# Kernel optimization log

Measured on AMD Instinct MI355X. Metric: run time of the kernel, lower is better.

## Reference

```python
import jax, jax.numpy as jnp
import numpy as np
from jax import lax

B = 256
WIDTH = 64
STRUCT = [512, 1024, 1024, 1000]
N_LAYERS = len(STRUCT) - 2  # LSTM layers (last pair is the classifier)


def setup_inputs() -> dict:
    key = jax.random.key(0)
    ks = list(jax.random.split(key, 2 + 4 * N_LAYERS))
    inp = {"x": jax.random.normal(ks[0], (B, STRUCT[0] * WIDTH), jnp.float32)}
    ki = 1
    for j in range(N_LAYERS):
        n_x, n_h = STRUCT[j], STRUCT[j + 1]
        n_v = n_h + n_x  # variants == 0: concat(h_prev, x)
        std = np.float32(np.sqrt(2.0 / (n_v + n_h)))
        for g in ["F", "I", "C", "O"]:
            inp[f"{g}{j}"] = jax.random.normal(ks[ki], (n_v, n_h), jnp.float32) * std
            ki += 1
        for g in ["bf", "bi", "bc", "bo"]:
            inp[f"{g}{j}"] = jnp.zeros((n_h,), jnp.float32)
    n_x, n_h = STRUCT[-2], STRUCT[-1]
    std = np.float32(np.sqrt(2.0 / (n_x + n_h)))
    inp["W"] = jax.random.normal(ks[ki], (n_x, n_h), jnp.float32) * std
    inp["b"] = jnp.zeros((n_h,), jnp.float32)
    return inp


def _lstm_forward(x, params, W, b):
    # x: [B, WIDTH*n_in] -> xs: [WIDTH, B, n_in] (tf.split along axis 1)
    bsz = x.shape[0]
    xs = x.reshape(bsz, WIDTH, STRUCT[0]).transpose(1, 0, 2)

    def step(carry, x_t):
        new_carry = []
        h = x_t
        for j, (F, I, C, O, bf, bi, bc, bo) in enumerate(params):
            c_f, h_f = carry[j]
            # variants==0: x_in = concat([h_prev, x]); k==0 sliced-weight path
            # equals zero h_prev/c_prev, so zero-init state is faithful.
            x_in = jnp.concatenate([h_f, h], axis=1)  # [B, n_h + n_x]
            f = jax.nn.sigmoid(x_in @ F + bf)
            i = jax.nn.sigmoid(x_in @ I + bi)
            c = f * c_f + i * jnp.tanh(x_in @ C + bc)
            o = jax.nn.sigmoid(x_in @ O + bo)
            h = o * jnp.tanh(c)
            new_carry.append((c, h))
        return tuple(new_carry), None

    init = tuple(
        (jnp.zeros((bsz, STRUCT[j + 1]), x.dtype), jnp.zeros((bsz, STRUCT[j + 1]), x.dtype))
        for j in range(N_LAYERS)
    )
    carry, _ = lax.scan(step, init, xs)
    h_last = carry[-1][1]  # top layer hidden at final timestep
    logits = h_last @ W + b
    pred = jax.nn.softmax(logits, axis=-1)
    return logits, pred


def reference(x, F0, I0, C0, O0, bf0, bi0, bc0, bo0,
              F1, I1, C1, O1, bf1, bi1, bc1, bo1, W, b):
    params = [
        (F0, I0, C0, O0, bf0, bi0, bc0, bo0),
        (F1, I1, C1, O1, bf1, bi1, bc1, bo1),
    ]
    return _lstm_forward(x, params, W, b)
```

## Files before the change

### kernel.cpp

```cpp
#include <hip/hip_runtime.h>
#include <hip/hip_bf16.h>


typedef short  bf16x8 __attribute__((ext_vector_type(8)));
typedef float  f32x4  __attribute__((ext_vector_type(4)));

#define NHID   1024
#define NBATCH 256
#define NBLK   256
#define HSZE   (NBATCH * NHID)

__device__ __forceinline__ unsigned short f2b(float f) {
    unsigned int u = __builtin_bit_cast(unsigned int, f);
    unsigned int r = (u + 0x7FFFu + ((u >> 16) & 1u)) >> 16;
    return (unsigned short)r;
}
__device__ __forceinline__ float sigmoidf_(float x) {
    return 1.0f / (1.0f + __expf(-x));
}
__device__ __forceinline__ float tanhf_(float x) {
    return 1.0f - 2.0f / (__expf(2.0f * x) + 1.0f);
}

__global__ __launch_bounds__(256)
void transpose_w_kernel(const float* __restrict__ w0, const float* __restrict__ w1,
                        const float* __restrict__ w2, const float* __restrict__ w3,
                        unsigned short* __restrict__ dst, int nv) {
    __shared__ unsigned short t[64][65];
    const int gate = blockIdx.z;
    const float* src = (gate == 0) ? w0 : (gate == 1) ? w1 : (gate == 2) ? w2 : w3;
    const int kt = blockIdx.x * 64;
    const int nt = blockIdx.y * 64;
    const int tid = threadIdx.x;
    const int rr = tid >> 6;
    const int cc = tid & 63;
    #pragma unroll
    for (int p = 0; p < 16; ++p) {
        const int row = p * 4 + rr;
        t[cc][row] = f2b(src[(size_t)(kt + row) * NHID + nt + cc]);
    }
    __syncthreads();
    #pragma unroll
    for (int p = 0; p < 16; ++p) {
        const int row = p * 4 + rr;
        dst[((size_t)gate * NHID + nt + row) * nv + kt + cc] = t[row][cc];
    }
}

__global__ __launch_bounds__(256)
void cvt_x_frag_kernel(const float* __restrict__ x, unsigned short* __restrict__ xb) {
    const int t  = blockIdx.x;
    const int mg = blockIdx.y;
    const int g  = threadIdx.x >> 6;
    const int l  = threadIdx.x & 63;
    const int row = l & 15, ko = l >> 4;
    const float* src = x + (size_t)(mg * 16 + row) * 32768 + t * 512 + ko * 8;
    unsigned short* dst = xb + ((size_t)t * 256 * 512) + ((size_t)mg * 16 * 64 + l) * 8;
    #pragma unroll
    for (int i = 0; i < 4; ++i) {
        const int c = g * 4 + i;
        const float4 v0 = *(const float4*)(src + (size_t)c * 32);
        const float4 v1 = *(const float4*)(src + (size_t)c * 32 + 4);
        ushort4 o0, o1;
        o0.x = f2b(v0.x); o0.y = f2b(v0.y); o0.z = f2b(v0.z); o0.w = f2b(v0.w);
        o1.x = f2b(v1.x); o1.y = f2b(v1.y); o1.z = f2b(v1.z); o1.w = f2b(v1.w);
        *(ushort4*)(dst + (size_t)c * 512)     = o0;
        *(ushort4*)(dst + (size_t)c * 512 + 4) = o1;
    }
}

__device__ __forceinline__ void grid_sync(unsigned* bar, unsigned gen) {
    __syncthreads();
    if (threadIdx.x == 0) {
        __builtin_amdgcn_fence(__ATOMIC_RELEASE, "agent");
        unsigned* grp  = bar + (blockIdx.x & 7) * 16;
        unsigned* glob = bar + 128;
        unsigned* gctr = bar + 144;
        if (__hip_atomic_fetch_add(grp, 1u, __ATOMIC_RELAXED, __HIP_MEMORY_SCOPE_AGENT)
                == gen * 32u + 31u) {
            if (__hip_atomic_fetch_add(glob, 1u, __ATOMIC_RELAXED, __HIP_MEMORY_SCOPE_AGENT)
                    == gen * 8u + 7u) {
                __hip_atomic_store(gctr, gen + 1u, __ATOMIC_RELAXED, __HIP_MEMORY_SCOPE_AGENT);
            }
        }
        while (__hip_atomic_load(gctr, __ATOMIC_RELAXED, __HIP_MEMORY_SCOPE_AGENT) <= gen) {
            __builtin_amdgcn_s_sleep(2);
        }
        __builtin_amdgcn_fence(__ATOMIC_ACQUIRE, "agent");
    }
    __syncthreads();
}

__global__ __launch_bounds__(512)
void lstm_persist_kernel(const unsigned short* __restrict__ wt0,
                         const unsigned short* __restrict__ wt1,
                         const unsigned short* __restrict__ xb,
                         const float* __restrict__ bf0, const float* __restrict__ bi0,
                         const float* __restrict__ bc0, const float* __restrict__ bo0,
                         const float* __restrict__ bf1, const float* __restrict__ bi1,
                         const float* __restrict__ bc1, const float* __restrict__ bo1,
                         unsigned short* __restrict__ h0b,
                         unsigned short* __restrict__ h1b,
                         float* __restrict__ h1f,
                         unsigned* __restrict__ bar) {
    __shared__ __align__(16) unsigned short lw[65536];

    const int tid  = threadIdx.x;
    const int lane = tid & 63;
    const int w    = tid >> 6;
    const int c15  = lane & 15;
    const int kg   = lane >> 4;
    const int b    = blockIdx.x;
    const int layer = (b >> 3) & 1;
    const int lb    = ((b >> 4) << 3) | (b & 7);

    const unsigned short* wt = layer ? wt1 : wt0;
    const int NV  = layer ? 2048 : 1536;
    const int NCW = NV >> 5;
    const int NX  = layer ? 32 : 16;

    #pragma unroll
    for (int i = 0; i < 8; ++i) {
        const int c = w + i * 8;
        if (c < NCW) {
            #pragma unroll
            for (int rt = 0; rt < 2; ++rt) {
                const int R   = rt * 16 + c15;
                const int g   = R >> 3;
                const int hid = 8 * lb + (R & 7);
                const int k   = c * 32 + kg * 8;
                *(bf16x8*)(lw + ((size_t)(c * 2 + rt) * 64 + lane) * 8) =
                    *(const bf16x8*)(wt + ((size_t)g * NHID + hid) * NV + k);
            }
        }
    }

    f32x4 biasv[2];
    {
        const float* bp[4];
        if (layer) { bp[0] = bf1; bp[1] = bi1; bp[2] = bc1; bp[3] = bo1; }
        else       { bp[0] = bf0; bp[1] = bi0; bp[2] = bc0; bp[3] = bo0; }
        #pragma unroll
        for (int rt = 0; rt < 2; ++rt)
            #pragma unroll
            for (int j = 0; j < 4; ++j) {
                const int R = rt * 16 + kg * 4 + j;
                biasv[rt][j] = bp[R >> 3][8 * lb + (R & 7)];
            }
    }
    __syncthreads();

    float cs[4] = {0.f, 0.f, 0.f, 0.f};
    unsigned gen = 0;

    const int rot_h = (b >> 3) & 31;
    const int rot_x = layer ? rot_h : ((b >> 4) & 15);
    const bool hiM  = (kg >= 2);

    const int chw = lb >> 2, kow = lb & 3, eb = (kg & 1) * 4;
    const int mg   = 2 * w + (hiM ? 1 : 0);
    const int mrow = 32 * w + (hiM ? 16 : 0) + c15;
    const size_t hoff = (((size_t)mg * 32 + chw) * 64 + kow * 16 + c15) * 8 + eb;

    auto step = [&](const unsigned short* bh, const unsigned short* bx,
                    unsigned short* hout, float* hfout) {
        f32x4 a00 = biasv[0], a01 = biasv[0];
        f32x4 a10 = biasv[1], a11 = biasv[1];
        const unsigned short* ph0 = bh + ((size_t)(2 * w)     * 32 * 64 + lane) * 8;
        const unsigned short* ph1 = bh + ((size_t)(2 * w + 1) * 32 * 64 + lane) * 8;
        const unsigned short* px0 = bx + ((size_t)(2 * w)     * NX * 64 + lane) * 8;
        const unsigned short* px1 = bx + ((size_t)(2 * w + 1) * NX * 64 + lane) * 8;

        #pragma unroll 8
        for (int i = 0; i < 32; ++i) {
            const int cc = (i + rot_h) & 31;
            const bf16x8 va0 = *(const bf16x8*)(lw + ((size_t)(cc * 2)     * 64 + lane) * 8);
            const bf16x8 va1 = *(const bf16x8*)(lw + ((size_t)(cc * 2 + 1) * 64 + lane) * 8);
            const bf16x8 vb0 = *(const bf16x8*)(ph0 + (size_t)cc * 512);
            const bf16x8 vb1 = *(const bf16x8*)(ph1 + (size_t)cc * 512);
            a00 = __builtin_amdgcn_mfma_f32_16x16x32_bf16(va0, vb0, a00, 0, 0, 0);
            a01 = __builtin_amdgcn_mfma_f32_16x16x32_bf16(va0, vb1, a01, 0, 0, 0);
            a10 = __builtin_amdgcn_mfma_f32_16x16x32_bf16(va1, vb0, a10, 0, 0, 0);
            a11 = __builtin_amdgcn_mfma_f32_16x16x32_bf16(va1, vb1, a11, 0, 0, 0);
        }
        #pragma unroll 8
        for (int i = 0; i < NX; ++i) {
            const int cc = (i + rot_x) & (NX - 1);
            const bf16x8 va0 = *(const bf16x8*)(lw + ((size_t)((32 + cc) * 2)     * 64 + lane) * 8);
            const bf16x8 va1 = *(const bf16x8*)(lw + ((size_t)((32 + cc) * 2 + 1) * 64 + lane) * 8);
            const bf16x8 vb0 = *(const bf16x8*)(px0 + (size_t)cc * 512);
            const bf16x8 vb1 = *(const bf16x8*)(px1 + (size_t)cc * 512);
            a00 = __builtin_amdgcn_mfma_f32_16x16x32_bf16(va0, vb0, a00, 0, 0, 0);
            a01 = __builtin_amdgcn_mfma_f32_16x16x32_bf16(va0, vb1, a01, 0, 0, 0);
            a10 = __builtin_amdgcn_mfma_f32_16x16x32_bf16(va1, vb0, a10, 0, 0, 0);
            a11 = __builtin_amdgcn_mfma_f32_16x16x32_bf16(va1, vb1, a11, 0, 0, 0);
        }

        f32x4 r0, r1;
        #pragma unroll
        for (int j = 0; j < 4; ++j) {
            const float s0 = hiM ? a01[j] : a00[j];
            const float s1 = hiM ? a11[j] : a10[j];
            const float t0 = __shfl_xor(a00[j], 32);
            const float t1 = __shfl_xor(a01[j], 32);
            const float t2 = __shfl_xor(a10[j], 32);
            const float t3 = __shfl_xor(a11[j], 32);
            r0[j] = hiM ? t1 : t0;
            r1[j] = hiM ? t3 : t2;
            (void)s0; (void)s1;
        }
        const f32x4 own0 = hiM ? a01 : a00;
        const f32x4 own1 = hiM ? a11 : a10;

        ushort4 hb;
        float4  hf;
        float hv[4];
        #pragma unroll
        for (int j = 0; j < 4; ++j) {
            const float fsv = hiM ? r0[j]   : own0[j];
            const float isv = hiM ? own0[j] : r0[j];
            const float csv = hiM ? r1[j]   : own1[j];
            const float osv = hiM ? own1[j] : r1[j];
            const float fv = sigmoidf_(fsv);
            const float iv = sigmoidf_(isv);
            const float cv = tanhf_(csv);
            const float ov = sigmoidf_(osv);
            const float ccv = fv * cs[j] + iv * cv;
            const float hh  = ov * tanhf_(ccv);
            cs[j] = ccv;
            hv[j] = hh;
        }
        hb.x = f2b(hv[0]); hb.y = f2b(hv[1]); hb.z = f2b(hv[2]); hb.w = f2b(hv[3]);
        *reinterpret_cast<ushort4*>(hout + hoff) = hb;
        if (hfout) {
            hf.x = hv[0]; hf.y = hv[1]; hf.z = hv[2]; hf.w = hv[3];
            *reinterpret_cast<float4*>(hfout + (size_t)mrow * NHID + 8 * lb + eb) = hf;
        }
    };

    for (int t = 0; t <= 64; ++t) {
        if (layer == 0) {
            if (t < 64) {
                step(h0b + (size_t)((t + 1) & 1) * HSZE,
                     xb + (size_t)t * 256 * 512,
                     h0b + (size_t)(t & 1) * HSZE, nullptr);
            }
        } else {
            if (t >= 1) {
                const int u = t - 1;
                step(h1b + (size_t)((u + 1) & 1) * HSZE,
                     h0b + (size_t)(u & 1) * HSZE,
                     h1b + (size_t)(u & 1) * HSZE,
                     (u == 63) ? h1f : nullptr);
            }
        }
        if (t < 64) {
            grid_sync(bar, gen);
            ++gen;
        }
    }
}

__global__ __launch_bounds__(256)
void classifier_kernel(const float* __restrict__ h, const float* __restrict__ W,
                       const float* __restrict__ b, float* __restrict__ logits) {
    __shared__ float hs[4 * 1024];
    const int tid = threadIdx.x;
    const int m0 = blockIdx.y * 4;
    const int n  = blockIdx.x * 256 + tid;
    #pragma unroll
    for (int i = 0; i < 16; ++i)
        hs[i * 256 + tid] = h[(size_t)m0 * NHID + i * 256 + tid];
    __syncthreads();
    if (n < 1000) {
        float a0 = 0.f, a1 = 0.f, a2 = 0.f, a3 = 0.f;
        #pragma unroll 8
        for (int k = 0; k < NHID; ++k) {
            const float wv = W[(size_t)k * 1000 + n];
            a0 = fmaf(hs[k], wv, a0);
            a1 = fmaf(hs[1024 + k], wv, a1);
            a2 = fmaf(hs[2048 + k], wv, a2);
            a3 = fmaf(hs[3072 + k], wv, a3);
        }
        const float bv = b[n];
        logits[(size_t)(m0 + 0) * 1000 + n] = a0 + bv;
        logits[(size_t)(m0 + 1) * 1000 + n] = a1 + bv;
        logits[(size_t)(m0 + 2) * 1000 + n] = a2 + bv;
        logits[(size_t)(m0 + 3) * 1000 + n] = a3 + bv;
    }
}

__global__ void softmax_kernel(const float* __restrict__ logits, float* __restrict__ pred) {
    __shared__ float red[256];
    const int m = blockIdx.x;
    const int t = threadIdx.x;
    const float* lr = logits + (size_t)m * 1000;
    float mx = -3.4e38f;
    for (int i = t; i < 1000; i += 256) mx = fmaxf(mx, lr[i]);
    red[t] = mx; __syncthreads();
    for (int off = 128; off > 0; off >>= 1) {
        if (t < off) red[t] = fmaxf(red[t], red[t + off]);
        __syncthreads();
    }
    mx = red[0];
    __syncthreads();
    float sm = 0.0f;
    for (int i = t; i < 1000; i += 256) sm += __expf(lr[i] - mx);
    red[t] = sm; __syncthreads();
    for (int off = 128; off > 0; off >>= 1) {
        if (t < off) red[t] += red[t + off];
        __syncthreads();
    }
    const float inv = 1.0f / red[0];
    for (int i = t; i < 1000; i += 256)
        pred[(size_t)m * 1000 + i] = __expf(lr[i] - mx) * inv;
}

extern "C" void kernel_launch(void* const* d_in, const int* in_sizes, int n_in,
                              void* d_out, int out_size, void* d_ws, size_t ws_size,
                              hipStream_t stream) {
    (void)in_sizes; (void)n_in; (void)out_size; (void)ws_size;
    const float* x = (const float*)d_in[0];
    const float* W0[4] = {(const float*)d_in[1], (const float*)d_in[2], (const float*)d_in[3], (const float*)d_in[4]};
    const float* B0[4] = {(const float*)d_in[5], (const float*)d_in[6], (const float*)d_in[7], (const float*)d_in[8]};
    const float* W1[4] = {(const float*)d_in[9], (const float*)d_in[10], (const float*)d_in[11], (const float*)d_in[12]};
    const float* B1[4] = {(const float*)d_in[13], (const float*)d_in[14], (const float*)d_in[15], (const float*)d_in[16]};
    const float* Wc = (const float*)d_in[17];
    const float* bc = (const float*)d_in[18];
    float* out = (float*)d_out;

    char* ws = (char*)d_ws;
    size_t off = 0;
    auto alloc = [&](size_t bytes) -> char* {
        char* p = ws + off;
        off += (bytes + 255) & ~(size_t)255;
        return p;
    };
    unsigned short* wt0 = (unsigned short*)alloc((size_t)4 * NHID * 1536 * 2);
    unsigned short* wt1 = (unsigned short*)alloc((size_t)4 * NHID * 2048 * 2);
    unsigned short* xb  = (unsigned short*)alloc((size_t)NBATCH * 64 * 512 * 2);
    char* hstates = ws + off;
    unsigned short* h0b = (unsigned short*)alloc((size_t)2 * HSZE * 2);
    unsigned short* h1b = (unsigned short*)alloc((size_t)2 * HSZE * 2);
    size_t hstate_bytes = (size_t)((char*)h1b + (size_t)2 * HSZE * 2 - hstates);
    float* h1f = (float*)alloc((size_t)HSZE * 4);
    unsigned* bar = (unsigned*)alloc(1024);

    hipMemsetAsync(hstates, 0, hstate_bytes, stream);
    hipMemsetAsync(bar, 0, 1024, stream);

    transpose_w_kernel<<<dim3(1536 / 64, 16, 4), 256, 0, stream>>>(
        W0[0], W0[1], W0[2], W0[3], wt0, 1536);
    transpose_w_kernel<<<dim3(2048 / 64, 16, 4), 256, 0, stream>>>(
        W1[0], W1[1], W1[2], W1[3], wt1, 2048);
    cvt_x_frag_kernel<<<dim3(64, 16), 256, 0, stream>>>(x, xb);

    lstm_persist_kernel<<<NBLK, 512, 0, stream>>>(
        wt0, wt1, xb,
        B0[0], B0[1], B0[2], B0[3],
        B1[0], B1[1], B1[2], B1[3],
        h0b, h1b, h1f, bar);

    classifier_kernel<<<dim3(4, 64), 256, 0, stream>>>(h1f, Wc, bc, out);
    softmax_kernel<<<NBATCH, 256, 0, stream>>>(out, out + (size_t)NBATCH * 1000);
}
```

Before: 1.488 ms.

## Split LSTM persistent kernel across 512 blocks with four hidden units each

Doubles the persistent grid from 256 to 512 blocks. Each block now owns 4 hidden units per gate instead of 8, which halves the LDS weight slice (64 KB) and the MFMA work per block. The gate exchange is reworked to a two-stage lane shuffle, and the grid barrier now uses 16 groups. The aim is to spread the recurrent GEMV over more CUs and shorten each timestep's critical path. The cost is more blocks in every grid sync, a heavier atomic barrier, and a requirement that all 512 blocks be co-resident, which the added launch_bounds occupancy hint targets.

```diff
diff --git a/kernel.cpp b/kernel.cpp
--- a/kernel.cpp
+++ b/kernel.cpp
@@ -7,7 +7,6 @@
 
 #define NHID   1024
 #define NBATCH 256
-#define NBLK   256
 #define HSZE   (NBATCH * NHID)
 
 __device__ __forceinline__ unsigned short f2b(float f) {
@@ -73,13 +72,13 @@
     __syncthreads();
     if (threadIdx.x == 0) {
         __builtin_amdgcn_fence(__ATOMIC_RELEASE, "agent");
-        unsigned* grp  = bar + (blockIdx.x & 7) * 16;
-        unsigned* glob = bar + 128;
-        unsigned* gctr = bar + 144;
+        unsigned* grp  = bar + (blockIdx.x & 15) * 16;
+        unsigned* glob = bar + 256;
+        unsigned* gctr = bar + 272;
         if (__hip_atomic_fetch_add(grp, 1u, __ATOMIC_RELAXED, __HIP_MEMORY_SCOPE_AGENT)
                 == gen * 32u + 31u) {
             if (__hip_atomic_fetch_add(glob, 1u, __ATOMIC_RELAXED, __HIP_MEMORY_SCOPE_AGENT)
-                    == gen * 8u + 7u) {
+                    == gen * 16u + 15u) {
                 __hip_atomic_store(gctr, gen + 1u, __ATOMIC_RELAXED, __HIP_MEMORY_SCOPE_AGENT);
             }
         }
@@ -91,7 +90,7 @@
     __syncthreads();
 }
 
-__global__ __launch_bounds__(512)
+__global__ __launch_bounds__(512, 4)
 void lstm_persist_kernel(const unsigned short* __restrict__ wt0,
                          const unsigned short* __restrict__ wt1,
                          const unsigned short* __restrict__ xb,
@@ -103,7 +102,7 @@
                          unsigned short* __restrict__ h1b,
                          float* __restrict__ h1f,
                          unsigned* __restrict__ bar) {
-    __shared__ __align__(16) unsigned short lw[65536];
+    __shared__ __align__(16) unsigned short lw[32768];
 
     const int tid  = threadIdx.x;
     const int lane = tid & 63;
@@ -117,55 +116,48 @@
     const unsigned short* wt = layer ? wt1 : wt0;
     const int NV  = layer ? 2048 : 1536;
     const int NCW = NV >> 5;
-    const int NX  = layer ? 32 : 16;
-
-    #pragma unroll
-    for (int i = 0; i < 8; ++i) {
-        const int c = w + i * 8;
-        if (c < NCW) {
-            #pragma unroll
-            for (int rt = 0; rt < 2; ++rt) {
-                const int R   = rt * 16 + c15;
-                const int g   = R >> 3;
-                const int hid = 8 * lb + (R & 7);
-                const int k   = c * 32 + kg * 8;
-                *(bf16x8*)(lw + ((size_t)(c * 2 + rt) * 64 + lane) * 8) =
-                    *(const bf16x8*)(wt + ((size_t)g * NHID + hid) * NV + k);
-            }
-        }
-    }
-
-    f32x4 biasv[2];
+
     {
-        const float* bp[4];
-        if (layer) { bp[0] = bf1; bp[1] = bi1; bp[2] = bc1; bp[3] = bo1; }
-        else       { bp[0] = bf0; bp[1] = bi0; bp[2] = bc0; bp[3] = bo0; }
+        const int g   = c15 >> 2;
+        const int hid = 4 * lb + (c15 & 3);
+        const unsigned short* s = wt + ((size_t)g * NHID + hid) * NV + kg * 8;
         #pragma unroll
-        for (int rt = 0; rt < 2; ++rt)
-            #pragma unroll
-            for (int j = 0; j < 4; ++j) {
-                const int R = rt * 16 + kg * 4 + j;
-                biasv[rt][j] = bp[R >> 3][8 * lb + (R & 7)];
-            }
-    }
-    __syncthreads();
-
-    float cs[4] = {0.f, 0.f, 0.f, 0.f};
+        for (int i = 0; i < 8; ++i) {
+            const int c = w + i * 8;
+            if (c < NCW)
+                *(bf16x8*)(lw + ((size_t)c * 64 + lane) * 8) = *(const bf16x8*)(s + c * 32);
+        }
+    }
+
+    f32x4 biasv;
+    {
+        const float* bg;
+        if (layer) bg = (kg == 0) ? bf1 : (kg == 1) ? bi1 : (kg == 2) ? bc1 : bo1;
+        else       bg = (kg == 0) ? bf0 : (kg == 1) ? bi0 : (kg == 2) ? bc0 : bo0;
+        const float4 v = *(const float4*)(bg + 4 * lb);
+        biasv[0] = v.x; biasv[1] = v.y; biasv[2] = v.z; biasv[3] = v.w;
+    }
+    __syncthreads();
+
+    float cs[2] = {0.f, 0.f};
     unsigned gen = 0;
 
-    const int rot_h = (b >> 3) & 31;
-    const int rot_x = layer ? rot_h : ((b >> 4) & 15);
-    const bool hiM  = (kg >= 2);
-
-    const int chw = lb >> 2, kow = lb & 3, eb = (kg & 1) * 4;
-    const int mg   = 2 * w + (hiM ? 1 : 0);
-    const int mrow = 32 * w + (hiM ? 16 : 0) + c15;
-    const size_t hoff = (((size_t)mg * 32 + chw) * 64 + kow * 16 + c15) * 8 + eb;
-
-    auto step = [&](const unsigned short* bh, const unsigned short* bx,
+    const int rot_h  = (b >> 4) & 31;
+    const int rot_xL = layer ? ((b >> 4) & 31) : ((b >> 4) & 15);
+
+    const int mf = (kg >> 1) & 1;
+    const int jp = 2 * (kg & 1);
+    const int mg   = 2 * w + mf;
+    const int mrow = 32 * w + 16 * mf + c15;
+    const int chw  = lb >> 3;
+    const int kow  = (lb >> 1) & 3;
+    const int eoff = 4 * (lb & 1) + jp;
+    const size_t hoff = (((size_t)mg * 32 + chw) * 64 + kow * 16 + c15) * 8 + eoff;
+
+    auto step = [&](const int NX, const int rot_x,
+                    const unsigned short* bh, const unsigned short* bx,
                     unsigned short* hout, float* hfout) {
-        f32x4 a00 = biasv[0], a01 = biasv[0];
-        f32x4 a10 = biasv[1], a11 = biasv[1];
+        f32x4 acc0 = biasv, acc1 = biasv;
         const unsigned short* ph0 = bh + ((size_t)(2 * w)     * 32 * 64 + lane) * 8;
         const unsigned short* ph1 = bh + ((size_t)(2 * w + 1) * 32 * 64 + lane) * 8;
         const unsigned short* px0 = bx + ((size_t)(2 * w)     * NX * 64 + lane) * 8;
@@ -174,81 +166,77 @@
         #pragma unroll 8
         for (int i = 0; i < 32; ++i) {
             const int cc = (i + rot_h) & 31;
-            const bf16x8 va0 = *(const bf16x8*)(lw + ((size_t)(cc * 2)     * 64 + lane) * 8);
-            const bf16x8 va1 = *(const bf16x8*)(lw + ((size_t)(cc * 2 + 1) * 64 + lane) * 8);
-            const bf16x8 vb0 = *(const bf16x8*)(ph0 + (size_t)cc * 512);
-            const bf16x8 vb1 = *(const bf16x8*)(ph1 + (size_t)cc * 512);
-            a00 = __builtin_amdgcn_mfma_f32_16x16x32_bf16(va0, vb0, a00, 0, 0, 0);
-            a01 = __builtin_amdgcn_mfma_f32_16x16x32_bf16(va0, vb1, a01, 0, 0, 0);
-            a10 = __builtin_amdgcn_mfma_f32_16x16x32_bf16(va1, vb0, a10, 0, 0, 0);
-            a11 = __builtin_amdgcn_mfma_f32_16x16x32_bf16(va1, vb1, a11, 0, 0, 0);
+            const bf16x8 va = *(const bf16x8*)(lw + ((size_t)cc * 64 + lane) * 8);
+            const bf16x8 b0 = *(const bf16x8*)(ph0 + (size_t)cc * 512);
+            const bf16x8 b1 = *(const bf16x8*)(ph1 + (size_t)cc * 512);
+            acc0 = __builtin_amdgcn_mfma_f32_16x16x32_bf16(va, b0, acc0, 0, 0, 0);
+            acc1 = __builtin_amdgcn_mfma_f32_16x16x32_bf16(va, b1, acc1, 0, 0, 0);
         }
         #pragma unroll 8
         for (int i = 0; i < NX; ++i) {
             const int cc = (i + rot_x) & (NX - 1);
-            const bf16x8 va0 = *(const bf16x8*)(lw + ((size_t)((32 + cc) * 2)     * 64 + lane) * 8);
-            const bf16x8 va1 = *(const bf16x8*)(lw + ((size_t)((32 + cc) * 2 + 1) * 64 + lane) * 8);
-            const bf16x8 vb0 = *(const bf16x8*)(px0 + (size_t)cc * 512);
-            const bf16x8 vb1 = *(const bf16x8*)(px1 + (size_t)cc * 512);
-            a00 = __builtin_amdgcn_mfma_f32_16x16x32_bf16(va0, vb0, a00, 0, 0, 0);
-            a01 = __builtin_amdgcn_mfma_f32_16x16x32_bf16(va0, vb1, a01, 0, 0, 0);
-            a10 = __builtin_amdgcn_mfma_f32_16x16x32_bf16(va1, vb0, a10, 0, 0, 0);
-            a11 = __builtin_amdgcn_mfma_f32_16x16x32_bf16(va1, vb1, a11, 0, 0, 0);
-        }
-
-        f32x4 r0, r1;
+            const bf16x8 va = *(const bf16x8*)(lw + ((size_t)(32 + cc) * 64 + lane) * 8);
+            const bf16x8 b0 = *(const bf16x8*)(px0 + (size_t)cc * 512);
+            const bf16x8 b1 = *(const bf16x8*)(px1 + (size_t)cc * 512);
+            acc0 = __builtin_amdgcn_mfma_f32_16x16x32_bf16(va, b0, acc0, 0, 0, 0);
+            acc1 = __builtin_amdgcn_mfma_f32_16x16x32_bf16(va, b1, acc1, 0, 0, 0);
+        }
+
+        f32x4 sendA = (kg & 2) ? acc0 : acc1;
+        f32x4 recvA;
         #pragma unroll
-        for (int j = 0; j < 4; ++j) {
-            const float s0 = hiM ? a01[j] : a00[j];
-            const float s1 = hiM ? a11[j] : a10[j];
-            const float t0 = __shfl_xor(a00[j], 32);
-            const float t1 = __shfl_xor(a01[j], 32);
-            const float t2 = __shfl_xor(a10[j], 32);
-            const float t3 = __shfl_xor(a11[j], 32);
-            r0[j] = hiM ? t1 : t0;
-            r1[j] = hiM ? t3 : t2;
-            (void)s0; (void)s1;
-        }
-        const f32x4 own0 = hiM ? a01 : a00;
-        const f32x4 own1 = hiM ? a11 : a10;
-
-        ushort4 hb;
-        float4  hf;
-        float hv[4];
+        for (int j = 0; j < 4; ++j) recvA[j] = __shfl_xor(sendA[j], 32);
+        const f32x4 mine = (kg & 2) ? acc1 : acc0;
+
+        const int jo = 2 * ((kg & 1) ^ 1);
+        const float g1_0 = __shfl_xor(mine[jo],      16);
+        const float g1_1 = __shfl_xor(mine[jo + 1],  16);
+        const float g3_0 = __shfl_xor(recvA[jo],     16);
+        const float g3_1 = __shfl_xor(recvA[jo + 1], 16);
+        const float m_0  = mine[jp],  m_1  = mine[jp + 1];
+        const float rA_0 = recvA[jp], rA_1 = recvA[jp + 1];
+
+        float hv[2];
         #pragma unroll
-        for (int j = 0; j < 4; ++j) {
-            const float fsv = hiM ? r0[j]   : own0[j];
-            const float isv = hiM ? own0[j] : r0[j];
-            const float csv = hiM ? r1[j]   : own1[j];
-            const float osv = hiM ? own1[j] : r1[j];
+        for (int jj = 0; jj < 2; ++jj) {
+            const float m_  = jj ? m_1  : m_0;
+            const float g1  = jj ? g1_1 : g1_0;
+            const float rA  = jj ? rA_1 : rA_0;
+            const float g3  = jj ? g3_1 : g3_0;
+            const float fsv = (kg == 0) ? m_ : (kg == 1) ? g1 : (kg == 2) ? rA : g3;
+            const float isv = (kg == 1) ? m_ : (kg == 0) ? g1 : (kg == 3) ? rA : g3;
+            const float csv = (kg == 2) ? m_ : (kg == 3) ? g1 : (kg == 0) ? rA : g3;
+            const float osv = (kg == 3) ? m_ : (kg == 2) ? g1 : (kg == 1) ? rA : g3;
             const float fv = sigmoidf_(fsv);
             const float iv = sigmoidf_(isv);
             const float cv = tanhf_(csv);
             const float ov = sigmoidf_(osv);
-            const float ccv = fv * cs[j] + iv * cv;
+            const float ccv = fv * cs[jj] + iv * cv;
             const float hh  = ov * tanhf_(ccv);
-            cs[j] = ccv;
-            hv[j] = hh;
-        }
-        hb.x = f2b(hv[0]); hb.y = f2b(hv[1]); hb.z = f2b(hv[2]); hb.w = f2b(hv[3]);
-        *reinterpret_cast<ushort4*>(hout + hoff) = hb;
+            cs[jj] = ccv;
+            hv[jj] = hh;
+        }
+        const unsigned hb = (unsigned)f2b(hv[0]) | ((unsigned)f2b(hv[1]) << 16);
+        *reinterpret_cast<unsigned*>(hout + hoff) = hb;
         if (hfout) {
-            hf.x = hv[0]; hf.y = hv[1]; hf.z = hv[2]; hf.w = hv[3];
-            *reinterpret_cast<float4*>(hfout + (size_t)mrow * NHID + 8 * lb + eb) = hf;
+            float2 hf; hf.x = hv[0]; hf.y = hv[1];
+            *reinterpret_cast<float2*>(hfout + (size_t)mrow * NHID + 4 * lb + jp) = hf;
         }
     };
 
     for (int t = 0; t <= 64; ++t) {
         if (layer == 0) {
             if (t < 64) {
-                step(h0b + (size_t)((t + 1) & 1) * HSZE,
+                step(16, rot_xL,
+                     h0b + (size_t)((t + 1) & 1) * HSZE,
                      xb + (size_t)t * 256 * 512,
                      h0b + (size_t)(t & 1) * HSZE, nullptr);
             }
         } else {
             if (t >= 1) {
                 const int u = t - 1;
-                step(h1b + (size_t)((u + 1) & 1) * HSZE,
+                step(32, rot_xL,
+                     h1b + (size_t)((u + 1) & 1) * HSZE,
                      h0b + (size_t)(u & 1) * HSZE,
                      h1b + (size_t)(u & 1) * HSZE,
                      (u == 63) ? h1f : nullptr);
@@ -344,10 +332,10 @@
     unsigned short* h1b = (unsigned short*)alloc((size_t)2 * HSZE * 2);
     size_t hstate_bytes = (size_t)((char*)h1b + (size_t)2 * HSZE * 2 - hstates);
     float* h1f = (float*)alloc((size_t)HSZE * 4);
-    unsigned* bar = (unsigned*)alloc(1024);
+    unsigned* bar = (unsigned*)alloc(2048);
 
     hipMemsetAsync(hstates, 0, hstate_bytes, stream);
-    hipMemsetAsync(bar, 0, 1024, stream);
+    hipMemsetAsync(bar, 0, 2048, stream);
 
     transpose_w_kernel<<<dim3(1536 / 64, 16, 4), 256, 0, stream>>>(
         W0[0], W0[1], W0[2], W0[3], wt0, 1536);
@@ -355,7 +343,7 @@
         W1[0], W1[1], W1[2], W1[3], wt1, 2048);
     cvt_x_frag_kernel<<<dim3(64, 16), 256, 0, stream>>>(x, xb);
 
-    lstm_persist_kernel<<<NBLK, 512, 0, stream>>>(
+    lstm_persist_kernel<<<512, 512, 0, stream>>>(
         wt0, wt1, xb,
         B0[0], B0[1], B0[2], B0[3],
         B1[0], B1[1], B1[2], B1[3],
```

Measured after the change: 2.497 ms. 1.68x slower.

## Double threads per block, each wave computing one 16-row batch tile

Applied to the files above, without the earlier changes.

The persistent LSTM kernel now launches 1024 threads per block instead of 512. Each of the 16 waves handles one 16-row batch slice with two MFMA accumulators, where each of the 8 waves previously handled two slices with four. The aim is more waves per CU to hide latency on the serial per-timestep chain and a shorter MFMA chain per wave. In exchange, each weight fragment read from LDS is reused across half as many batch columns, LDS traffic per block roughly doubles, and the cell-update work is now split so each lane keeps two cell states instead of four.

```diff
diff --git a/kernel.cpp b/kernel.cpp
--- a/kernel.cpp
+++ b/kernel.cpp
@@ -91,7 +91,7 @@
     __syncthreads();
 }
 
-__global__ __launch_bounds__(512)
+__global__ __launch_bounds__(1024, 4)
 void lstm_persist_kernel(const unsigned short* __restrict__ wt0,
                          const unsigned short* __restrict__ wt1,
                          const unsigned short* __restrict__ xb,
@@ -117,11 +117,10 @@
     const unsigned short* wt = layer ? wt1 : wt0;
     const int NV  = layer ? 2048 : 1536;
     const int NCW = NV >> 5;
-    const int NX  = layer ? 32 : 16;
-
-    #pragma unroll
-    for (int i = 0; i < 8; ++i) {
-        const int c = w + i * 8;
+
+    #pragma unroll
+    for (int i = 0; i < 4; ++i) {
+        const int c = w + i * 16;
         if (c < NCW) {
             #pragma unroll
             for (int rt = 0; rt < 2; ++rt) {
@@ -150,105 +149,90 @@
     }
     __syncthreads();
 
-    float cs[4] = {0.f, 0.f, 0.f, 0.f};
+    float cs[2] = {0.f, 0.f};
     unsigned gen = 0;
 
-    const int rot_h = (b >> 3) & 31;
-    const int rot_x = layer ? rot_h : ((b >> 4) & 15);
-    const bool hiM  = (kg >= 2);
-
-    const int chw = lb >> 2, kow = lb & 3, eb = (kg & 1) * 4;
-    const int mg   = 2 * w + (hiM ? 1 : 0);
-    const int mrow = 32 * w + (hiM ? 16 : 0) + c15;
-    const size_t hoff = (((size_t)mg * 32 + chw) * 64 + kow * 16 + c15) * 8 + eb;
-
-    auto step = [&](const unsigned short* bh, const unsigned short* bx,
+    const int rot_h  = (b >> 3) & 31;
+    const int rot_xL = layer ? rot_h : ((b >> 4) & 15);
+
+    const int hb4  = 4 * (kg & 1);
+    const int jsel = (kg >> 1) ? 2 : 0;
+    const int hp   = hb4 + jsel;
+    const int mrow = 16 * w + c15;
+    const int chw  = lb >> 2;
+    const int kow  = lb & 3;
+    const size_t hoff = (((size_t)w * 32 + chw) * 64 + kow * 16 + c15) * 8 + hp;
+
+    auto step = [&](const int NX, const int rot_x,
+                    const unsigned short* bh, const unsigned short* bx,
                     unsigned short* hout, float* hfout) {
-        f32x4 a00 = biasv[0], a01 = biasv[0];
-        f32x4 a10 = biasv[1], a11 = biasv[1];
-        const unsigned short* ph0 = bh + ((size_t)(2 * w)     * 32 * 64 + lane) * 8;
-        const unsigned short* ph1 = bh + ((size_t)(2 * w + 1) * 32 * 64 + lane) * 8;
-        const unsigned short* px0 = bx + ((size_t)(2 * w)     * NX * 64 + lane) * 8;
-        const unsigned short* px1 = bx + ((size_t)(2 * w + 1) * NX * 64 + lane) * 8;
+        f32x4 acc0 = biasv[0], acc1 = biasv[1];
+        const unsigned short* ph = bh + ((size_t)w * 32 * 64 + lane) * 8;
+        const unsigned short* px = bx + ((size_t)w * NX * 64 + lane) * 8;
 
         #pragma unroll 8
         for (int i = 0; i < 32; ++i) {
             const int cc = (i + rot_h) & 31;
+            const bf16x8 vb  = *(const bf16x8*)(ph + (size_t)cc * 512);
             const bf16x8 va0 = *(const bf16x8*)(lw + ((size_t)(cc * 2)     * 64 + lane) * 8);
             const bf16x8 va1 = *(const bf16x8*)(lw + ((size_t)(cc * 2 + 1) * 64 + lane) * 8);
-            const bf16x8 vb0 = *(const bf16x8*)(ph0 + (size_t)cc * 512);
-            const bf16x8 vb1 = *(const bf16x8*)(ph1 + (size_t)cc * 512);
-            a00 = __builtin_amdgcn_mfma_f32_16x16x32_bf16(va0, vb0, a00, 0, 0, 0);
-            a01 = __builtin_amdgcn_mfma_f32_16x16x32_bf16(va0, vb1, a01, 0, 0, 0);
-            a10 = __builtin_amdgcn_mfma_f32_16x16x32_bf16(va1, vb0, a10, 0, 0, 0);
-            a11 = __builtin_amdgcn_mfma_f32_16x16x32_bf16(va1, vb1, a11, 0, 0, 0);
+            acc0 = __builtin_amdgcn_mfma_f32_16x16x32_bf16(va0, vb, acc0, 0, 0, 0);
+            acc1 = __builtin_amdgcn_mfma_f32_16x16x32_bf16(va1, vb, acc1, 0, 0, 0);
         }
         #pragma unroll 8
         for (int i = 0; i < NX; ++i) {
             const int cc = (i + rot_x) & (NX - 1);
+            const bf16x8 vb  = *(const bf16x8*)(px + (size_t)cc * 512);
             const bf16x8 va0 = *(const bf16x8*)(lw + ((size_t)((32 + cc) * 2)     * 64 + lane) * 8);
             const bf16x8 va1 = *(const bf16x8*)(lw + ((size_t)((32 + cc) * 2 + 1) * 64 + lane) * 8);
-            const bf16x8 vb0 = *(const bf16x8*)(px0 + (size_t)cc * 512);
-            const bf16x8 vb1 = *(const bf16x8*)(px1 + (size_t)cc * 512);
-            a00 = __builtin_amdgcn_mfma_f32_16x16x32_bf16(va0, vb0, a00, 0, 0, 0);
-            a01 = __builtin_amdgcn_mfma_f32_16x16x32_bf16(va0, vb1, a01, 0, 0, 0);
-            a10 = __builtin_amdgcn_mfma_f32_16x16x32_bf16(va1, vb0, a10, 0, 0, 0);
-            a11 = __builtin_amdgcn_mfma_f32_16x16x32_bf16(va1, vb1, a11, 0, 0, 0);
-        }
-
-        f32x4 r0, r1;
+            acc0 = __builtin_amdgcn_mfma_f32_16x16x32_bf16(va0, vb, acc0, 0, 0, 0);
+            acc1 = __builtin_amdgcn_mfma_f32_16x16x32_bf16(va1, vb, acc1, 0, 0, 0);
+        }
+
+        f32x4 racc0, racc1;
         #pragma unroll
         for (int j = 0; j < 4; ++j) {
-            const float s0 = hiM ? a01[j] : a00[j];
-            const float s1 = hiM ? a11[j] : a10[j];
-            const float t0 = __shfl_xor(a00[j], 32);
-            const float t1 = __shfl_xor(a01[j], 32);
-            const float t2 = __shfl_xor(a10[j], 32);
-            const float t3 = __shfl_xor(a11[j], 32);
-            r0[j] = hiM ? t1 : t0;
-            r1[j] = hiM ? t3 : t2;
-            (void)s0; (void)s1;
-        }
-        const f32x4 own0 = hiM ? a01 : a00;
-        const f32x4 own1 = hiM ? a11 : a10;
-
-        ushort4 hb;
-        float4  hf;
-        float hv[4];
+            racc0[j] = __shfl_xor(acc0[j], 32);
+            racc1[j] = __shfl_xor(acc1[j], 32);
+        }
+
+        float hv[2];
         #pragma unroll
-        for (int j = 0; j < 4; ++j) {
-            const float fsv = hiM ? r0[j]   : own0[j];
-            const float isv = hiM ? own0[j] : r0[j];
-            const float csv = hiM ? r1[j]   : own1[j];
-            const float osv = hiM ? own1[j] : r1[j];
+        for (int jj = 0; jj < 2; ++jj) {
+            const int j = jsel + jj;
+            float fsv, isv, csv, osv;
+            if (kg < 2) { fsv = acc0[j];  isv = racc0[j]; csv = acc1[j];  osv = racc1[j]; }
+            else        { fsv = racc0[j]; isv = acc0[j];  csv = racc1[j]; osv = acc1[j];  }
             const float fv = sigmoidf_(fsv);
             const float iv = sigmoidf_(isv);
             const float cv = tanhf_(csv);
             const float ov = sigmoidf_(osv);
-            const float ccv = fv * cs[j] + iv * cv;
+            const float ccv = fv * cs[jj] + iv * cv;
             const float hh  = ov * tanhf_(ccv);
-            cs[j] = ccv;
-            hv[j] = hh;
-        }
-        hb.x = f2b(hv[0]); hb.y = f2b(hv[1]); hb.z = f2b(hv[2]); hb.w = f2b(hv[3]);
-        *reinterpret_cast<ushort4*>(hout + hoff) = hb;
+            cs[jj] = ccv;
+            hv[jj] = hh;
+        }
+        const unsigned hbp = (unsigned)f2b(hv[0]) | ((unsigned)f2b(hv[1]) << 16);
+        *reinterpret_cast<unsigned*>(hout + hoff) = hbp;
         if (hfout) {
-            hf.x = hv[0]; hf.y = hv[1]; hf.z = hv[2]; hf.w = hv[3];
-            *reinterpret_cast<float4*>(hfout + (size_t)mrow * NHID + 8 * lb + eb) = hf;
+            float2 hf; hf.x = hv[0]; hf.y = hv[1];
+            *reinterpret_cast<float2*>(hfout + (size_t)mrow * NHID + 8 * lb + hp) = hf;
         }
     };
 
     for (int t = 0; t <= 64; ++t) {
         if (layer == 0) {
             if (t < 64) {
-                step(h0b + (size_t)((t + 1) & 1) * HSZE,
+                step(16, rot_xL,
+                     h0b + (size_t)((t + 1) & 1) * HSZE,
                      xb + (size_t)t * 256 * 512,
                      h0b + (size_t)(t & 1) * HSZE, nullptr);
             }
         } else {
             if (t >= 1) {
                 const int u = t - 1;
-                step(h1b + (size_t)((u + 1) & 1) * HSZE,
+                step(32, rot_xL,
+                     h1b + (size_t)((u + 1) & 1) * HSZE,
                      h0b + (size_t)(u & 1) * HSZE,
                      h1b + (size_t)(u & 1) * HSZE,
                      (u == 63) ? h1f : nullptr);
@@ -355,7 +339,7 @@
         W1[0], W1[1], W1[2], W1[3], wt1, 2048);
     cvt_x_frag_kernel<<<dim3(64, 16), 256, 0, stream>>>(x, xb);
 
-    lstm_persist_kernel<<<NBLK, 512, 0, stream>>>(
+    lstm_persist_kernel<<<NBLK, 1024, 0, stream>>>(
         wt0, wt1, xb,
         B0[0], B0[1], B0[2], B0[3],
         B1[0], B1[1], B1[2], B1[3],
```

Measured after the change: 1.435 ms. 3.6% less time.
